# Kernel tuning notes

Hardware: AMD Instinct MI355X
Metric: run time of the kernel (lower is better)

## Reference

```python
import jax, jax.numpy as jnp
import numpy as np

HIDDEN = 246


def _gcn_conv(x, W, b, src, dst, norm, n_nodes):
    # PyG GCNConv: linear (no bias) -> normalized neighbor aggregation -> + bias
    h = x @ W                                   # [N, C_out]
    msg = h[src] * norm[:, None]                # [E', C_out]
    agg = jax.ops.segment_sum(msg, dst, num_segments=n_nodes)
    return agg + b


def setup_inputs() -> dict:
    key = jax.random.key(0)
    ks = jax.random.split(key, 10)
    N, F_IN, E = 50000, 256, 320000
    x = jax.random.normal(ks[0], (N, F_IN), dtype=jnp.float32)
    edge_index = jax.random.randint(ks[1], (2, E), 0, N, dtype=jnp.int64)
    def glorot(k, fan_in, fan_out):
        s = jnp.sqrt(2.0 / (fan_in + fan_out)).astype(jnp.float32)
        return jax.random.normal(k, (fan_in, fan_out), dtype=jnp.float32) * s
    return {
        "x": x,
        "edge_index": edge_index,
        "W1": glorot(ks[2], F_IN, HIDDEN), "b1": jnp.zeros((HIDDEN,), jnp.float32),
        "W2": glorot(ks[3], HIDDEN, HIDDEN), "b2": jnp.zeros((HIDDEN,), jnp.float32),
        "W3": glorot(ks[4], HIDDEN, HIDDEN), "b3": jnp.zeros((HIDDEN,), jnp.float32),
        "W4": glorot(ks[5], HIDDEN, HIDDEN), "b4": jnp.zeros((HIDDEN,), jnp.float32),
    }


def reference(x, edge_index, W1, b1, W2, b2, W3, b3, W4, b4):
    N = x.shape[0]
    src, dst = edge_index[0], edge_index[1]
    # add self-loops (edge_weight=None -> all-ones weights)
    loops = jnp.arange(N, dtype=edge_index.dtype)
    src_f = jnp.concatenate([src, loops])
    dst_f = jnp.concatenate([dst, loops])
    # symmetric GCN normalization: D^{-1/2} (A+I) D^{-1/2}
    deg = jax.ops.segment_sum(jnp.ones_like(src_f, dtype=x.dtype), dst_f, num_segments=N)
    dinv = jnp.where(deg > 0, jax.lax.rsqrt(jnp.maximum(deg, 1.0)), 0.0)
    norm = dinv[src_f] * dinv[dst_f]            # [E+N]

    h = jax.nn.relu(_gcn_conv(x, W1, b1, src_f, dst_f, norm, N))
    h = jax.nn.relu(_gcn_conv(h, W2, b2, src_f, dst_f, norm, N))
    h = jax.nn.relu(_gcn_conv(h, W3, b3, src_f, dst_f, norm, N))
    h = _gcn_conv(h, W4, b4, src_f, dst_f, norm, N)
    # NOTE: original forward never calls conv5; log_softmax over hidden dim,
    # faithfully reproduced. Dropout is identity in eval mode.
    return jax.nn.log_softmax(h, axis=1)
```

## Files before the change

kernel.cpp:

```cpp
#include <hip/hip_runtime.h>
#include <cstdint>
#include <cstddef>


typedef __bf16 bf16x8 __attribute__((ext_vector_type(8)));
typedef float f32x4 __attribute__((ext_vector_type(4)));

__device__ __forceinline__ unsigned short f2bf(float v) {
    union { float f; unsigned u; } x; x.f = v;
    unsigned r = x.u + 0x7fff + ((x.u >> 16) & 1);
    return (unsigned short)(r >> 16);
}
__device__ __forceinline__ float bf2f(unsigned short h) {
    union { unsigned u; float f; } x; x.u = (unsigned)h << 16; return x.f;
}

__device__ __forceinline__ void gl2lds16(const void* g, void* l) {
    __builtin_amdgcn_global_load_lds(
        (const __attribute__((address_space(1))) unsigned int*)g,
        (__attribute__((address_space(3))) unsigned int*)l, 16, 0, 0);
}

__device__ __forceinline__ void fma4(const uint2 v, float n, float* acc) {
    acc[0] += bf2f((unsigned short)(v.x & 0xffff)) * n;
    acc[1] += bf2f((unsigned short)(v.x >> 16)) * n;
    acc[2] += bf2f((unsigned short)(v.y & 0xffff)) * n;
    acc[3] += bf2f((unsigned short)(v.y >> 16)) * n;
}

__global__ void k_flag_init(int* flag) {
    if (blockIdx.x == 0 && threadIdx.x == 0) *flag = 1;
}

__global__ void k_flag_check(const long long* __restrict__ p, int E, long long N,
                             int* flag) {
    long long i = (long long)blockIdx.x * blockDim.x + threadIdx.x;
    long long stride = (long long)gridDim.x * blockDim.x;
    for (; i < E; i += stride) {
        long long v = p[i];
        if (v < 0 || v >= N) *flag = 0;
    }
}

__device__ __forceinline__ void load_edge(const void* eidx, int fl, int E, int i,
                                          int& s, int& d) {
    if (fl) {
        s = (int)((const long long*)eidx)[i];
        d = (int)((const long long*)eidx)[E + i];
    } else {
        s = ((const int*)eidx)[i];
        d = ((const int*)eidx)[E + i];
    }
}

__global__ void k_zero_i32(int* __restrict__ p, int n) {
    int i = blockIdx.x * blockDim.x + threadIdx.x;
    if (i < n) p[i] = 0;
}

__global__ void k_count(const void* __restrict__ eidx, const int* __restrict__ flag,
                        int* __restrict__ counts, int E) {
    int i = blockIdx.x * blockDim.x + threadIdx.x;
    if (i >= E) return;
    int s, d;
    load_edge(eidx, *flag, E, i, s, d);
    atomicAdd(&counts[d], 1);
}

__global__ void k_dinv(const int* __restrict__ counts, float* __restrict__ dinv,
                       int N) {
    int i = blockIdx.x * blockDim.x + threadIdx.x;
    if (i < N) dinv[i] = rsqrtf((float)counts[i] + 1.0f);
}

__global__ __launch_bounds__(256) void k_bsum(const int* __restrict__ counts,
                                              int* __restrict__ bsum, int N) {
    __shared__ int ws[4];
    int tid = threadIdx.x, lane = tid & 63, wid = tid >> 6;
    int base = blockIdx.x * 1024 + tid * 4;
    int s = 0;
    if (base + 3 < N) {
        int4 v = *(const int4*)&counts[base];
        s = v.x + v.y + v.z + v.w;
    } else {
#pragma unroll
        for (int t = 0; t < 4; t++) {
            int i = base + t;
            if (i < N) s += counts[i];
        }
    }
#pragma unroll
    for (int off = 32; off > 0; off >>= 1) s += __shfl_xor(s, off);
    if (lane == 0) ws[wid] = s;
    __syncthreads();
    if (tid == 0) bsum[blockIdx.x] = ws[0] + ws[1] + ws[2] + ws[3];
}

__global__ __launch_bounds__(1024) void k_scan(const int* __restrict__ counts,
                                               int* __restrict__ starts, int N) {
    __shared__ int wsum[16];
    __shared__ int wscan[16];
    __shared__ int s_carry;
    int tid = threadIdx.x;
    int lane = tid & 63, wid = tid >> 6;
    if (tid == 0) s_carry = 0;
    __syncthreads();
    for (int base = 0; base < N; base += 1024) {
        int i = base + tid;
        int v = (i < N) ? counts[i] : 0;
        int incl = v;
#pragma unroll
        for (int off = 1; off < 64; off <<= 1) {
            int t = __shfl_up(incl, off);
            if (lane >= off) incl += t;
        }
        if (lane == 63) wsum[wid] = incl;
        __syncthreads();
        if (wid == 0 && lane < 16) {
            int w = wsum[lane];
#pragma unroll
            for (int off = 1; off < 16; off <<= 1) {
                int t = __shfl_up(w, off);
                if (lane >= off) w += t;
            }
            wscan[lane] = w;
        }
        __syncthreads();
        int woff = (wid > 0) ? wscan[wid - 1] : 0;
        int excl = s_carry + woff + incl - v;
        if (i < N) starts[i] = excl;
        int total = wscan[15];
        __syncthreads();
        if (tid == 0) s_carry += total;
        __syncthreads();
    }
    if (tid == 0) starts[N] = s_carry;
}

__global__ __launch_bounds__(256) void k_scan_final(
        const int* __restrict__ counts, const int* __restrict__ boffs,
        int* __restrict__ starts, int N) {
    __shared__ int ws[4];
    int tid = threadIdx.x, lane = tid & 63, wid = tid >> 6;
    int base = blockIdx.x * 1024 + tid * 4;
    int v[4];
#pragma unroll
    for (int t = 0; t < 4; t++) {
        int i = base + t;
        v[t] = (i < N) ? counts[i] : 0;
    }
    int tsum = v[0] + v[1] + v[2] + v[3];
    int incl = tsum;
#pragma unroll
    for (int off = 1; off < 64; off <<= 1) {
        int t = __shfl_up(incl, off);
        if (lane >= off) incl += t;
    }
    if (lane == 63) ws[wid] = incl;
    __syncthreads();
    int woff = 0;
#pragma unroll
    for (int w = 0; w < 4; w++)
        if (w < wid) woff += ws[w];
    int run = boffs[blockIdx.x] + woff + incl - tsum;
#pragma unroll
    for (int t = 0; t < 4; t++) {
        int i = base + t;
        if (i < N) starts[i] = run;
        run += v[t];
    }
    if (blockIdx.x == 0 && tid == 0) starts[N] = boffs[gridDim.x];
}

__global__ void k_copy_i32(const int* __restrict__ a, int* __restrict__ b, int n) {
    int i = blockIdx.x * blockDim.x + threadIdx.x;
    if (i < n) b[i] = a[i];
}

__global__ void k_fill(const void* __restrict__ eidx, const int* __restrict__ flag,
                       int* __restrict__ cursor, int* __restrict__ srcs,
                       float* __restrict__ nrm, const float* __restrict__ dinv,
                       int E) {
    int i = blockIdx.x * blockDim.x + threadIdx.x;
    if (i >= E) return;
    int s, d;
    load_edge(eidx, *flag, E, i, s, d);
    int pos = atomicAdd(&cursor[d], 1);
    srcs[pos] = s;
    nrm[pos] = dinv[s];
}

__global__ void k_cvt_x(const float* __restrict__ x, unsigned short* __restrict__ o,
                        long long n4) {
    long long i = (long long)blockIdx.x * blockDim.x + threadIdx.x;
    long long stride = (long long)gridDim.x * blockDim.x;
    for (; i < n4; i += stride) {
        float4 v = ((const float4*)x)[i];
        unsigned a = (unsigned)f2bf(v.x) | ((unsigned)f2bf(v.y) << 16);
        unsigned b = (unsigned)f2bf(v.z) | ((unsigned)f2bf(v.w) << 16);
        ((uint2*)o)[i] = make_uint2(a, b);
    }
}

__global__ void k_cvt_w(const float* __restrict__ W, unsigned short* __restrict__ T,
                        int K, int H) {
    int idx = blockIdx.x * blockDim.x + threadIdx.x;
    if (idx >= 256 * 256) return;
    int k = idx & 255, n = idx >> 8;
    float v = (k < K && n < H) ? W[k * H + n] : 0.0f;
    T[n * 256 + k] = f2bf(v);
}

__global__ __launch_bounds__(256) void k_gemm_mfma(
        const unsigned short* __restrict__ A,
        const unsigned short* __restrict__ BT,
        unsigned short* __restrict__ C, int M) {
    __shared__ unsigned short ldsA[4 * 128 * 8];
    __shared__ unsigned short ldsB[4 * 128 * 8];

    int g = blockIdx.x, nwg = gridDim.x;
    int q = nwg >> 3, r = nwg & 7;
    int xcd = g & 7, slot = g >> 3;
    int work = (xcd < r) ? xcd * (q + 1) + slot
                         : r * (q + 1) + (xcd - r) * q + slot;
    int col0 = (work & 1) * 128;
    int row0 = (work >> 1) * 128;

    int tid = threadIdx.x;
    int lane = tid & 63;
    int w = tid >> 6;
    int wm = (w & 1) * 64, wn = (w >> 1) * 64;
    int kq = lane >> 4, lr = lane & 15;

    f32x4 acc[4][4] = {};

    for (int k0 = 0; k0 < 256; k0 += 32) {
        __syncthreads();
#pragma unroll
        for (int i = 0; i < 2; i++) {
            int c = (i * 4 + w) * 64 + lane;
            int m = c & 127, kqq = c >> 7;
            int row = row0 + m; if (row >= M) row = M - 1;
            gl2lds16(&A[(long long)row * 256 + k0 + kqq * 8],
                     &ldsA[(i * 4 + w) * 512]);
        }
#pragma unroll
        for (int i = 0; i < 2; i++) {
            int c = (i * 4 + w) * 64 + lane;
            int n = c & 127, kqq = c >> 7;
            gl2lds16(&BT[(long long)(col0 + n) * 256 + k0 + kqq * 8],
                     &ldsB[(i * 4 + w) * 512]);
        }
        __syncthreads();

        bf16x8 a[4], b[4];
#pragma unroll
        for (int t = 0; t < 4; t++) {
            int m = wm + t * 16 + lr;
            a[t] = *(const bf16x8*)&ldsA[(kq * 128 + m) * 8];
            int n = wn + t * 16 + lr;
            b[t] = *(const bf16x8*)&ldsB[(kq * 128 + n) * 8];
        }
#pragma unroll
        for (int mt = 0; mt < 4; mt++)
#pragma unroll
            for (int nt = 0; nt < 4; nt++)
                acc[mt][nt] = __builtin_amdgcn_mfma_f32_16x16x32_bf16(
                    a[mt], b[nt], acc[mt][nt], 0, 0, 0);
    }

#pragma unroll
    for (int mt = 0; mt < 4; mt++) {
#pragma unroll
        for (int nt = 0; nt < 4; nt++) {
            int col = col0 + wn + nt * 16 + lr;
            int rowb = row0 + wm + mt * 16 + kq * 4;
#pragma unroll
            for (int r2 = 0; r2 < 4; r2++) {
                int row = rowb + r2;
                if (row < M) C[(long long)row * 256 + col] = f2bf(acc[mt][nt][r2]);
            }
        }
    }
}

__device__ __forceinline__ void agg_rows(
        const unsigned short* __restrict__ h,
        const int* __restrict__ srcs, const float* __restrict__ nrm,
        const int* __restrict__ starts, int d, int f0, float dd, float* acc) {
    int lane = threadIdx.x & 63;
    int e0 = starts[d], e1 = starts[d + 1];
    int cnt = e1 - e0;
    int cpre = cnt < 64 ? cnt : 64;

    acc[0] = acc[1] = acc[2] = acc[3] = 0.0f;
    {
        uint2 v = *(const uint2*)&h[((long long)d << 8) + f0];
        fma4(v, dd, acc);
    }
    int sv = 0; float nv = 0.0f;
    if (lane < cpre) { sv = srcs[e0 + lane]; nv = nrm[e0 + lane]; }

    for (int base = 0; base < cpre; base += 8) {
        uint2 vv[8]; float nn[8];
#pragma unroll
        for (int t = 0; t < 8; t++) {
            int j = base + t;
            int s = __shfl(sv, j);
            float n = __shfl(nv, j);
            if (j >= cpre) { s = d; n = 0.0f; }
            nn[t] = n;
            vv[t] = *(const uint2*)&h[((long long)s << 8) + f0];
        }
#pragma unroll
        for (int t = 0; t < 8; t++) fma4(vv[t], nn[t], acc);
    }
    for (int e = e0 + 64; e < e1; e++) {
        int s0 = srcs[e];
        float n0 = nrm[e];
        uint2 v0 = *(const uint2*)&h[((long long)s0 << 8) + f0];
        fma4(v0, n0, acc);
    }
}

__global__ __launch_bounds__(256) void k_gather_bf16(
        const unsigned short* __restrict__ h,
        const int* __restrict__ srcs, const float* __restrict__ nrm,
        const int* __restrict__ starts,
        const float* __restrict__ dinv, const float* __restrict__ bias,
        unsigned short* __restrict__ out, int N, int H) {
    int d = blockIdx.x * 4 + (threadIdx.x >> 6);
    if (d >= N) return;
    int lane = threadIdx.x & 63;
    int f0 = lane * 4;
    float dd = dinv[d];

    float acc[4];
    agg_rows(h, srcs, nrm, starts, d, f0, dd, acc);

    unsigned short o[4];
#pragma unroll
    for (int t = 0; t < 4; t++) {
        int f = f0 + t;
        float bb = (f < H) ? bias[f] : 0.0f;
        float v = fmaxf(acc[t] * dd + bb, 0.0f);
        o[t] = f2bf(v);
    }
    unsigned o01 = (unsigned)o[0] | ((unsigned)o[1] << 16);
    unsigned o23 = (unsigned)o[2] | ((unsigned)o[3] << 16);
    *(uint2*)&out[((long long)d << 8) + f0] = make_uint2(o01, o23);
}

__global__ __launch_bounds__(256) void k_gather_lsm(
        const unsigned short* __restrict__ h,
        const int* __restrict__ srcs, const float* __restrict__ nrm,
        const int* __restrict__ starts,
        const float* __restrict__ dinv, const float* __restrict__ bias,
        float* __restrict__ out, int N, int H) {
    int d = blockIdx.x * 4 + (threadIdx.x >> 6);
    if (d >= N) return;
    int lane = threadIdx.x & 63;
    int f0 = lane * 4;
    float dd = dinv[d];

    float acc[4];
    agg_rows(h, srcs, nrm, starts, d, f0, dd, acc);

    float v[4];
    float m = -INFINITY;
#pragma unroll
    for (int t = 0; t < 4; t++) {
        int f = f0 + t;
        float bb = (f < H) ? bias[f] : 0.0f;
        v[t] = acc[t] * dd + bb;
        if (f < H) m = fmaxf(m, v[t]);
    }
#pragma unroll
    for (int off = 32; off > 0; off >>= 1) m = fmaxf(m, __shfl_xor(m, off));
    float s = 0.0f;
#pragma unroll
    for (int t = 0; t < 4; t++) {
        int f = f0 + t;
        if (f < H) s += __expf(v[t] - m);
    }
#pragma unroll
    for (int off = 32; off > 0; off >>= 1) s += __shfl_xor(s, off);
    float lse = m + logf(s);
#pragma unroll
    for (int t = 0; t < 4; t++) {
        int f = f0 + t;
        if (f < H) out[(long long)d * H + f] = v[t] - lse;
    }
}

extern "C" void kernel_launch(void* const* d_in, const int* in_sizes, int n_in,
                              void* d_out, int out_size, void* d_ws, size_t ws_size,
                              hipStream_t stream) {
    const float* x    = (const float*)d_in[0];
    const void*  eidx = d_in[1];
    const float* W[4] = {(const float*)d_in[2], (const float*)d_in[4],
                         (const float*)d_in[6], (const float*)d_in[8]};
    const float* b[4] = {(const float*)d_in[3], (const float*)d_in[5],
                         (const float*)d_in[7], (const float*)d_in[9]};

    const int H   = in_sizes[3];
    const int E   = in_sizes[1] / 2;
    const int FIN = in_sizes[2] / H;
    const int N   = in_sizes[0] / FIN;

    auto align = [](size_t v) { return (v + 255) / 256 * 256; };
    char* ws = (char*)d_ws;
    size_t off = 0;
    int* flag = (int*)(ws + off);             off += 256;
    float* dinv = (float*)(ws + off);         off += align((size_t)N * 4);
    int* counts = (int*)(ws + off);           off += align((size_t)N * 4);
    int* starts = (int*)(ws + off);           off += align((size_t)(N + 1) * 4);
    int* srcs = (int*)(ws + off);             off += align((size_t)E * 4);
    float* nrm = (float*)(ws + off);          off += align((size_t)E * 4);
    int nb2 = (N + 1023) / 1024;
    int* bsum = (int*)(ws + off);             off += align((size_t)(nb2 + 1) * 4);
    int* boffs = (int*)(ws + off);            off += align((size_t)(nb2 + 1) * 4);
    unsigned short* Wt[4];
    for (int l = 0; l < 4; l++) {
        Wt[l] = (unsigned short*)(ws + off);  off += 256 * 256 * 2;
    }
    size_t actB = align((size_t)N * 256 * 2);
    unsigned short* A0 = (unsigned short*)(ws + off);  off += actB;
    unsigned short* A1 = (unsigned short*)(ws + off);  off += actB;
    unsigned short* Cb = (unsigned short*)(ws + off);  off += actB;

    int nb = (N + 255) / 256, eb = (E + 255) / 256;

    k_flag_init<<<1, 64, 0, stream>>>(flag);
    k_flag_check<<<512, 256, 0, stream>>>((const long long*)eidx, E, (long long)N, flag);

    k_zero_i32<<<nb, 256, 0, stream>>>(counts, N);
    k_count<<<eb, 256, 0, stream>>>(eidx, flag, counts, E);
    k_dinv<<<nb, 256, 0, stream>>>(counts, dinv, N);
    k_bsum<<<nb2, 256, 0, stream>>>(counts, bsum, N);
    k_scan<<<1, 1024, 0, stream>>>(bsum, boffs, nb2);
    k_scan_final<<<nb2, 256, 0, stream>>>(counts, boffs, starts, N);
    k_copy_i32<<<nb, 256, 0, stream>>>(starts, counts, N);
    k_fill<<<eb, 256, 0, stream>>>(eidx, flag, counts, srcs, nrm, dinv, E);

    k_cvt_w<<<256, 256, 0, stream>>>(W[0], Wt[0], FIN, H);
    for (int l = 1; l < 4; l++)
        k_cvt_w<<<256, 256, 0, stream>>>(W[l], Wt[l], H, H);
    k_cvt_x<<<1024, 256, 0, stream>>>(x, A0, (long long)N * FIN / 4);

    int ggrid = 2 * ((N + 127) / 128);
    int gb = (N + 3) / 4;

    k_gemm_mfma<<<ggrid, 256, 0, stream>>>(A0, Wt[0], Cb, N);
    k_gather_bf16<<<gb, 256, 0, stream>>>(Cb, srcs, nrm, starts, dinv, b[0], A1, N, H);
    k_gemm_mfma<<<ggrid, 256, 0, stream>>>(A1, Wt[1], Cb, N);
    k_gather_bf16<<<gb, 256, 0, stream>>>(Cb, srcs, nrm, starts, dinv, b[1], A0, N, H);
    k_gemm_mfma<<<ggrid, 256, 0, stream>>>(A0, Wt[2], Cb, N);
    k_gather_bf16<<<gb, 256, 0, stream>>>(Cb, srcs, nrm, starts, dinv, b[2], A1, N, H);
    k_gemm_mfma<<<ggrid, 256, 0, stream>>>(A1, Wt[3], Cb, N);
    k_gather_lsm<<<gb, 256, 0, stream>>>(Cb, srcs, nrm, starts, dinv, b[3],
                                         (float*)d_out, N, H);
}
```

Before: 421.6 us.

## Fuse neighbor aggregation with next layer's GEMM through LDS

Replaces the separate gather kernel and following GEMM for layers 2-4 with one kernel. Each 512-thread block aggregates 128 destination rows into a swizzled 64KB LDS tile, then runs bf16 MFMA against the transposed weights with B read directly from global memory. This removes the round trip of the intermediate activation through HBM and two kernel launches per layer. In exchange, occupancy is limited by the 64KB LDS per block, gather latency can no longer be hidden by many small blocks, and the grid shrinks to about 391 blocks with a full N-tile computed per block.

```diff
diff --git a/kernel.cpp b/kernel.cpp
--- a/kernel.cpp
+++ b/kernel.cpp
@@ -323,32 +323,83 @@
     }
 }
 
-__global__ __launch_bounds__(256) void k_gather_bf16(
+__global__ __launch_bounds__(512, 4) void k_fused(
         const unsigned short* __restrict__ h,
         const int* __restrict__ srcs, const float* __restrict__ nrm,
-        const int* __restrict__ starts,
-        const float* __restrict__ dinv, const float* __restrict__ bias,
-        unsigned short* __restrict__ out, int N, int H) {
-    int d = blockIdx.x * 4 + (threadIdx.x >> 6);
-    if (d >= N) return;
-    int lane = threadIdx.x & 63;
+        const int* __restrict__ starts, const float* __restrict__ dinv,
+        const float* __restrict__ bias,
+        const unsigned short* __restrict__ BT,
+        unsigned short* __restrict__ C,
+        int N, int H) {
+    __shared__ unsigned short ldsA[128 * 256];
+
+    int tid = threadIdx.x;
+    int lane = tid & 63;
+    int w = tid >> 6;
+    int row0 = blockIdx.x * 128;
+
     int f0 = lane * 4;
-    float dd = dinv[d];
-
-    float acc[4];
-    agg_rows(h, srcs, nrm, starts, d, f0, dd, acc);
-
-    unsigned short o[4];
-#pragma unroll
-    for (int t = 0; t < 4; t++) {
-        int f = f0 + t;
-        float bb = (f < H) ? bias[f] : 0.0f;
-        float v = fmaxf(acc[t] * dd + bb, 0.0f);
-        o[t] = f2bf(v);
-    }
-    unsigned o01 = (unsigned)o[0] | ((unsigned)o[1] << 16);
-    unsigned o23 = (unsigned)o[2] | ((unsigned)o[3] << 16);
-    *(uint2*)&out[((long long)d << 8) + f0] = make_uint2(o01, o23);
+    for (int i = 0; i < 16; i++) {
+        int dl = w * 16 + i;
+        int d = row0 + dl;
+        if (d < N) {
+            float dd = dinv[d];
+            float acc[4];
+            agg_rows(h, srcs, nrm, starts, d, f0, dd, acc);
+            unsigned short o[4];
+#pragma unroll
+            for (int t = 0; t < 4; t++) {
+                int f = f0 + t;
+                float bb = (f < H) ? bias[f] : 0.0f;
+                float v = fmaxf(acc[t] * dd + bb, 0.0f);
+                o[t] = f2bf(v);
+            }
+            unsigned o01 = (unsigned)o[0] | ((unsigned)o[1] << 16);
+            unsigned o23 = (unsigned)o[2] | ((unsigned)o[3] << 16);
+            unsigned boff = (unsigned)(dl * 512 + lane * 8) ^
+                            (((unsigned)dl & 7u) << 4);
+            *(uint2*)((char*)ldsA + boff) = make_uint2(o01, o23);
+        }
+    }
+    __syncthreads();
+
+    int wm = (w & 1) * 64, wn = (w >> 1) * 64;
+    int kq = lane >> 4, lr = lane & 15;
+    f32x4 acc[4][4] = {};
+
+#pragma unroll
+    for (int k0 = 0; k0 < 256; k0 += 32) {
+        bf16x8 a[4], b[4];
+#pragma unroll
+        for (int t = 0; t < 4; t++) {
+            int row = wm + t * 16 + lr;
+            unsigned boff = (unsigned)(row * 512 + k0 * 2 + kq * 16) ^
+                            (((unsigned)row & 7u) << 4);
+            a[t] = *(const bf16x8*)((const char*)ldsA + boff);
+            int n = wn + t * 16 + lr;
+            b[t] = *(const bf16x8*)&BT[(long long)n * 256 + k0 + kq * 8];
+        }
+#pragma unroll
+        for (int mt = 0; mt < 4; mt++)
+#pragma unroll
+            for (int nt = 0; nt < 4; nt++)
+                acc[mt][nt] = __builtin_amdgcn_mfma_f32_16x16x32_bf16(
+                    a[mt], b[nt], acc[mt][nt], 0, 0, 0);
+    }
+
+#pragma unroll
+    for (int mt = 0; mt < 4; mt++) {
+#pragma unroll
+        for (int nt = 0; nt < 4; nt++) {
+            int col = wn + nt * 16 + lr;
+            int rowb = row0 + wm + mt * 16 + kq * 4;
+#pragma unroll
+            for (int r2 = 0; r2 < 4; r2++) {
+                int row = rowb + r2;
+                if (row < N) C[(long long)row * 256 + col] = f2bf(acc[mt][nt][r2]);
+            }
+        }
+    }
 }
 
 __global__ __launch_bounds__(256) void k_gather_lsm(
@@ -425,9 +476,9 @@
         Wt[l] = (unsigned short*)(ws + off);  off += 256 * 256 * 2;
     }
     size_t actB = align((size_t)N * 256 * 2);
-    unsigned short* A0 = (unsigned short*)(ws + off);  off += actB;
-    unsigned short* A1 = (unsigned short*)(ws + off);  off += actB;
-    unsigned short* Cb = (unsigned short*)(ws + off);  off += actB;
+    unsigned short* A0  = (unsigned short*)(ws + off);  off += actB;
+    unsigned short* Cb0 = (unsigned short*)(ws + off);  off += actB;
+    unsigned short* Cb1 = (unsigned short*)(ws + off);  off += actB;
 
     int nb = (N + 255) / 256, eb = (E + 255) / 256;
 
@@ -449,15 +500,16 @@
     k_cvt_x<<<1024, 256, 0, stream>>>(x, A0, (long long)N * FIN / 4);
 
     int ggrid = 2 * ((N + 127) / 128);
+    int fgrid = (N + 127) / 128;
     int gb = (N + 3) / 4;
 
-    k_gemm_mfma<<<ggrid, 256, 0, stream>>>(A0, Wt[0], Cb, N);
-    k_gather_bf16<<<gb, 256, 0, stream>>>(Cb, srcs, nrm, starts, dinv, b[0], A1, N, H);
-    k_gemm_mfma<<<ggrid, 256, 0, stream>>>(A1, Wt[1], Cb, N);
-    k_gather_bf16<<<gb, 256, 0, stream>>>(Cb, srcs, nrm, starts, dinv, b[1], A0, N, H);
-    k_gemm_mfma<<<ggrid, 256, 0, stream>>>(A0, Wt[2], Cb, N);
-    k_gather_bf16<<<gb, 256, 0, stream>>>(Cb, srcs, nrm, starts, dinv, b[2], A1, N, H);
-    k_gemm_mfma<<<ggrid, 256, 0, stream>>>(A1, Wt[3], Cb, N);
-    k_gather_lsm<<<gb, 256, 0, stream>>>(Cb, srcs, nrm, starts, dinv, b[3],
+    k_gemm_mfma<<<ggrid, 256, 0, stream>>>(A0, Wt[0], Cb0, N);
+    k_fused<<<fgrid, 512, 0, stream>>>(Cb0, srcs, nrm, starts, dinv, b[0],
+                                       Wt[1], Cb1, N, H);
+    k_fused<<<fgrid, 512, 0, stream>>>(Cb1, srcs, nrm, starts, dinv, b[1],
+                                       Wt[2], Cb0, N, H);
+    k_fused<<<fgrid, 512, 0, stream>>>(Cb0, srcs, nrm, starts, dinv, b[2],
+                                       Wt[3], Cb1, N, H);
+    k_gather_lsm<<<gb, 256, 0, stream>>>(Cb1, srcs, nrm, starts, dinv, b[3],
                                          (float*)d_out, N, H);
 }
```

Result: slower. 431.9 us (+2.4%).

## Process two nodes per wavefront in gather and fuse small setup kernels

Applied to the files above, without the earlier changes.

The gather kernels now map each 64-lane wavefront to two destination nodes, with 32 lanes each loading 8 bf16 features (16-byte loads) instead of 4, which halves the block count and widens the memory accesses. Several small preprocessing kernels are merged: zeroing goes into the flag check, dinv into the block-sum, the cursor copy into the scan-final pass, and the four weight conversions into one 2D launch. This cuts launch overhead and the number of passes over the count arrays. The risk is divergence when the two nodes sharing a wavefront have different degrees, and the inline edge prefetch now covers only 32 edges before falling back to serial loads.

```diff
diff --git a/kernel.cpp b/kernel.cpp
--- a/kernel.cpp
+++ b/kernel.cpp
@@ -21,11 +21,15 @@
         (__attribute__((address_space(3))) unsigned int*)l, 16, 0, 0);
 }
 
-__device__ __forceinline__ void fma4(const uint2 v, float n, float* acc) {
+__device__ __forceinline__ void fma8(const uint4 v, float n, float* acc) {
     acc[0] += bf2f((unsigned short)(v.x & 0xffff)) * n;
     acc[1] += bf2f((unsigned short)(v.x >> 16)) * n;
     acc[2] += bf2f((unsigned short)(v.y & 0xffff)) * n;
     acc[3] += bf2f((unsigned short)(v.y >> 16)) * n;
+    acc[4] += bf2f((unsigned short)(v.z & 0xffff)) * n;
+    acc[5] += bf2f((unsigned short)(v.z >> 16)) * n;
+    acc[6] += bf2f((unsigned short)(v.w & 0xffff)) * n;
+    acc[7] += bf2f((unsigned short)(v.w >> 16)) * n;
 }
 
 __global__ void k_flag_init(int* flag) {
@@ -33,9 +37,10 @@
 }
 
 __global__ void k_flag_check(const long long* __restrict__ p, int E, long long N,
-                             int* flag) {
+                             int* flag, int* __restrict__ counts, int Ncnt) {
     long long i = (long long)blockIdx.x * blockDim.x + threadIdx.x;
     long long stride = (long long)gridDim.x * blockDim.x;
+    for (long long j = i; j < Ncnt; j += stride) counts[j] = 0;
     for (; i < E; i += stride) {
         long long v = p[i];
         if (v < 0 || v >= N) *flag = 0;
@@ -53,11 +58,6 @@
     }
 }
 
-__global__ void k_zero_i32(int* __restrict__ p, int n) {
-    int i = blockIdx.x * blockDim.x + threadIdx.x;
-    if (i < n) p[i] = 0;
-}
-
 __global__ void k_count(const void* __restrict__ eidx, const int* __restrict__ flag,
                         int* __restrict__ counts, int E) {
     int i = blockIdx.x * blockDim.x + threadIdx.x;
@@ -67,28 +67,20 @@
     atomicAdd(&counts[d], 1);
 }
 
-__global__ void k_dinv(const int* __restrict__ counts, float* __restrict__ dinv,
-                       int N) {
-    int i = blockIdx.x * blockDim.x + threadIdx.x;
-    if (i < N) dinv[i] = rsqrtf((float)counts[i] + 1.0f);
-}
-
-__global__ __launch_bounds__(256) void k_bsum(const int* __restrict__ counts,
-                                              int* __restrict__ bsum, int N) {
+__global__ __launch_bounds__(256) void k_dinv_bsum(
+        const int* __restrict__ counts, float* __restrict__ dinv,
+        int* __restrict__ bsum, int N) {
     __shared__ int ws[4];
     int tid = threadIdx.x, lane = tid & 63, wid = tid >> 6;
     int base = blockIdx.x * 1024 + tid * 4;
-    int s = 0;
-    if (base + 3 < N) {
-        int4 v = *(const int4*)&counts[base];
-        s = v.x + v.y + v.z + v.w;
-    } else {
-#pragma unroll
-        for (int t = 0; t < 4; t++) {
-            int i = base + t;
-            if (i < N) s += counts[i];
-        }
-    }
+    int v[4];
+#pragma unroll
+    for (int t = 0; t < 4; t++) {
+        int i = base + t;
+        v[t] = (i < N) ? counts[i] : 0;
+        if (i < N) dinv[i] = rsqrtf((float)v[t] + 1.0f);
+    }
+    int s = v[0] + v[1] + v[2] + v[3];
 #pragma unroll
     for (int off = 32; off > 0; off >>= 1) s += __shfl_xor(s, off);
     if (lane == 0) ws[wid] = s;
@@ -138,7 +130,7 @@
 }
 
 __global__ __launch_bounds__(256) void k_scan_final(
-        const int* __restrict__ counts, const int* __restrict__ boffs,
+        int* __restrict__ counts, const int* __restrict__ boffs,
         int* __restrict__ starts, int N) {
     __shared__ int ws[4];
     int tid = threadIdx.x, lane = tid & 63, wid = tid >> 6;
@@ -166,15 +158,10 @@
 #pragma unroll
     for (int t = 0; t < 4; t++) {
         int i = base + t;
-        if (i < N) starts[i] = run;
+        if (i < N) { starts[i] = run; counts[i] = run; }
         run += v[t];
     }
     if (blockIdx.x == 0 && tid == 0) starts[N] = boffs[gridDim.x];
-}
-
-__global__ void k_copy_i32(const int* __restrict__ a, int* __restrict__ b, int n) {
-    int i = blockIdx.x * blockDim.x + threadIdx.x;
-    if (i < n) b[i] = a[i];
 }
 
 __global__ void k_fill(const void* __restrict__ eidx, const int* __restrict__ flag,
@@ -202,8 +189,15 @@
     }
 }
 
-__global__ void k_cvt_w(const float* __restrict__ W, unsigned short* __restrict__ T,
-                        int K, int H) {
+__global__ void k_cvt_w4(const float* __restrict__ W0, const float* __restrict__ W1,
+                         const float* __restrict__ W2, const float* __restrict__ W3,
+                         unsigned short* __restrict__ T0, unsigned short* __restrict__ T1,
+                         unsigned short* __restrict__ T2, unsigned short* __restrict__ T3,
+                         int K0, int K123, int H) {
+    int l = blockIdx.y;
+    const float* W = (l == 0) ? W0 : (l == 1) ? W1 : (l == 2) ? W2 : W3;
+    unsigned short* T = (l == 0) ? T0 : (l == 1) ? T1 : (l == 2) ? T2 : T3;
+    int K = (l == 0) ? K0 : K123;
     int idx = blockIdx.x * blockDim.x + threadIdx.x;
     if (idx >= 256 * 256) return;
     int k = idx & 255, n = idx >> 8;
@@ -284,42 +278,48 @@
     }
 }
 
-__device__ __forceinline__ void agg_rows(
+__device__ __forceinline__ void agg_rows2(
         const unsigned short* __restrict__ h,
         const int* __restrict__ srcs, const float* __restrict__ nrm,
         const int* __restrict__ starts, int d, int f0, float dd, float* acc) {
     int lane = threadIdx.x & 63;
+    int lr = lane & 31;
     int e0 = starts[d], e1 = starts[d + 1];
     int cnt = e1 - e0;
-    int cpre = cnt < 64 ? cnt : 64;
-
-    acc[0] = acc[1] = acc[2] = acc[3] = 0.0f;
+    int cpre = cnt < 32 ? cnt : 32;
+
+#pragma unroll
+    for (int t = 0; t < 8; t++) acc[t] = 0.0f;
     {
-        uint2 v = *(const uint2*)&h[((long long)d << 8) + f0];
-        fma4(v, dd, acc);
-    }
-    int sv = 0; float nv = 0.0f;
-    if (lane < cpre) { sv = srcs[e0 + lane]; nv = nrm[e0 + lane]; }
-
-    for (int base = 0; base < cpre; base += 8) {
-        uint2 vv[8]; float nn[8];
+        uint4 v = *(const uint4*)&h[((long long)d << 8) + f0];
+        fma8(v, dd, acc);
+    }
+    int sv = d; float nv = 0.0f;
+    if (lr < cpre) { sv = srcs[e0 + lr]; nv = nrm[e0 + lr]; }
+
+    int cother = __shfl(cpre, lane ^ 32);
+    int cmax = cpre > cother ? cpre : cother;
+
+    for (int base = 0; base < cmax; base += 8) {
+        uint4 vv[8]; float nn[8];
 #pragma unroll
         for (int t = 0; t < 8; t++) {
             int j = base + t;
-            int s = __shfl(sv, j);
-            float n = __shfl(nv, j);
+            int idx = (lane & 32) | j;
+            int s = __shfl(sv, idx);
+            float n = __shfl(nv, idx);
             if (j >= cpre) { s = d; n = 0.0f; }
             nn[t] = n;
-            vv[t] = *(const uint2*)&h[((long long)s << 8) + f0];
-        }
-#pragma unroll
-        for (int t = 0; t < 8; t++) fma4(vv[t], nn[t], acc);
-    }
-    for (int e = e0 + 64; e < e1; e++) {
+            vv[t] = *(const uint4*)&h[((long long)s << 8) + f0];
+        }
+#pragma unroll
+        for (int t = 0; t < 8; t++) fma8(vv[t], nn[t], acc);
+    }
+    for (int e = e0 + 32; e < e1; e++) {
         int s0 = srcs[e];
         float n0 = nrm[e];
-        uint2 v0 = *(const uint2*)&h[((long long)s0 << 8) + f0];
-        fma4(v0, n0, acc);
+        uint4 v0 = *(const uint4*)&h[((long long)s0 << 8) + f0];
+        fma8(v0, n0, acc);
     }
 }
 
@@ -329,26 +329,35 @@
         const int* __restrict__ starts,
         const float* __restrict__ dinv, const float* __restrict__ bias,
         unsigned short* __restrict__ out, int N, int H) {
-    int d = blockIdx.x * 4 + (threadIdx.x >> 6);
-    if (d >= N) return;
-    int lane = threadIdx.x & 63;
-    int f0 = lane * 4;
+    int tid = threadIdx.x;
+    int lane = tid & 63;
+    int g = (lane >> 5);
+    int lr = lane & 31;
+    int d = blockIdx.x * 8 + (tid >> 6) * 2 + g;
+    int gvalid = (d < N);
+    if (d >= N) d = N - 1;
+    int f0 = lr * 8;
     float dd = dinv[d];
 
-    float acc[4];
-    agg_rows(h, srcs, nrm, starts, d, f0, dd, acc);
-
-    unsigned short o[4];
-#pragma unroll
-    for (int t = 0; t < 4; t++) {
+    float acc[8];
+    agg_rows2(h, srcs, nrm, starts, d, f0, dd, acc);
+
+    unsigned short o[8];
+#pragma unroll
+    for (int t = 0; t < 8; t++) {
         int f = f0 + t;
         float bb = (f < H) ? bias[f] : 0.0f;
         float v = fmaxf(acc[t] * dd + bb, 0.0f);
         o[t] = f2bf(v);
     }
-    unsigned o01 = (unsigned)o[0] | ((unsigned)o[1] << 16);
-    unsigned o23 = (unsigned)o[2] | ((unsigned)o[3] << 16);
-    *(uint2*)&out[((long long)d << 8) + f0] = make_uint2(o01, o23);
+    if (gvalid) {
+        uint4 ov;
+        ov.x = (unsigned)o[0] | ((unsigned)o[1] << 16);
+        ov.y = (unsigned)o[2] | ((unsigned)o[3] << 16);
+        ov.z = (unsigned)o[4] | ((unsigned)o[5] << 16);
+        ov.w = (unsigned)o[6] | ((unsigned)o[7] << 16);
+        *(uint4*)&out[((long long)d << 8) + f0] = ov;
+    }
 }
 
 __global__ __launch_bounds__(256) void k_gather_lsm(
@@ -357,39 +366,45 @@
         const int* __restrict__ starts,
         const float* __restrict__ dinv, const float* __restrict__ bias,
         float* __restrict__ out, int N, int H) {
-    int d = blockIdx.x * 4 + (threadIdx.x >> 6);
-    if (d >= N) return;
-    int lane = threadIdx.x & 63;
-    int f0 = lane * 4;
+    int tid = threadIdx.x;
+    int lane = tid & 63;
+    int g = (lane >> 5);
+    int lr = lane & 31;
+    int d = blockIdx.x * 8 + (tid >> 6) * 2 + g;
+    int gvalid = (d < N);
+    if (d >= N) d = N - 1;
+    int f0 = lr * 8;
     float dd = dinv[d];
 
-    float acc[4];
-    agg_rows(h, srcs, nrm, starts, d, f0, dd, acc);
-
-    float v[4];
+    float acc[8];
+    agg_rows2(h, srcs, nrm, starts, d, f0, dd, acc);
+
+    float v[8];
     float m = -INFINITY;
 #pragma unroll
-    for (int t = 0; t < 4; t++) {
+    for (int t = 0; t < 8; t++) {
         int f = f0 + t;
         float bb = (f < H) ? bias[f] : 0.0f;
         v[t] = acc[t] * dd + bb;
         if (f < H) m = fmaxf(m, v[t]);
     }
 #pragma unroll
-    for (int off = 32; off > 0; off >>= 1) m = fmaxf(m, __shfl_xor(m, off));
+    for (int off = 16; off > 0; off >>= 1) m = fmaxf(m, __shfl_xor(m, off));
     float s = 0.0f;
 #pragma unroll
-    for (int t = 0; t < 4; t++) {
+    for (int t = 0; t < 8; t++) {
         int f = f0 + t;
         if (f < H) s += __expf(v[t] - m);
     }
 #pragma unroll
-    for (int off = 32; off > 0; off >>= 1) s += __shfl_xor(s, off);
+    for (int off = 16; off > 0; off >>= 1) s += __shfl_xor(s, off);
     float lse = m + logf(s);
-#pragma unroll
-    for (int t = 0; t < 4; t++) {
-        int f = f0 + t;
-        if (f < H) out[(long long)d * H + f] = v[t] - lse;
+    if (gvalid) {
+#pragma unroll
+        for (int t = 0; t < 8; t++) {
+            int f = f0 + t;
+            if (f < H) out[(long long)d * H + f] = v[t] - lse;
+        }
     }
 }
 
@@ -429,27 +444,25 @@
     unsigned short* A1 = (unsigned short*)(ws + off);  off += actB;
     unsigned short* Cb = (unsigned short*)(ws + off);  off += actB;
 
-    int nb = (N + 255) / 256, eb = (E + 255) / 256;
+    int eb = (E + 255) / 256;
 
     k_flag_init<<<1, 64, 0, stream>>>(flag);
-    k_flag_check<<<512, 256, 0, stream>>>((const long long*)eidx, E, (long long)N, flag);
-
-    k_zero_i32<<<nb, 256, 0, stream>>>(counts, N);
+    k_flag_check<<<512, 256, 0, stream>>>((const long long*)eidx, E, (long long)N,
+                                          flag, counts, N);
+
     k_count<<<eb, 256, 0, stream>>>(eidx, flag, counts, E);
-    k_dinv<<<nb, 256, 0, stream>>>(counts, dinv, N);
-    k_bsum<<<nb2, 256, 0, stream>>>(counts, bsum, N);
+    k_dinv_bsum<<<nb2, 256, 0, stream>>>(counts, dinv, bsum, N);
     k_scan<<<1, 1024, 0, stream>>>(bsum, boffs, nb2);
     k_scan_final<<<nb2, 256, 0, stream>>>(counts, boffs, starts, N);
-    k_copy_i32<<<nb, 256, 0, stream>>>(starts, counts, N);
     k_fill<<<eb, 256, 0, stream>>>(eidx, flag, counts, srcs, nrm, dinv, E);
 
-    k_cvt_w<<<256, 256, 0, stream>>>(W[0], Wt[0], FIN, H);
-    for (int l = 1; l < 4; l++)
-        k_cvt_w<<<256, 256, 0, stream>>>(W[l], Wt[l], H, H);
+    k_cvt_w4<<<dim3(256, 4), 256, 0, stream>>>(W[0], W[1], W[2], W[3],
+                                               Wt[0], Wt[1], Wt[2], Wt[3],
+                                               FIN, H, H);
     k_cvt_x<<<1024, 256, 0, stream>>>(x, A0, (long long)N * FIN / 4);
 
     int ggrid = 2 * ((N + 127) / 128);
-    int gb = (N + 3) / 4;
+    int gb = (N + 7) / 8;
 
     k_gemm_mfma<<<ggrid, 256, 0, stream>>>(A0, Wt[0], Cb, N);
     k_gather_bf16<<<gb, 256, 0, stream>>>(Cb, srcs, nrm, starts, dinv, b[0], A1, N, H);
```

After: 455.0 us. +7.9%, slower.
